# Optimization experiments

Measured on AMD Instinct MI355X. Metric: run time of the kernel, lower is better.

Reference implementation:

```python
import jax, jax.numpy as jnp
import numpy as np

N = 100000      # nodes
E = 1600000     # edges
G = 64          # graphs in batch
IN_CH = 2
HID = 64
HEADS = 4
TASKS = 2
NEG_SLOPE = 0.2  # PyG GATConv default leaky-relu slope


def gat_conv(x, src, dst, W, att_src, att_dst, bias, heads, out_ch, concat):
    """PyG-style GATConv (eval mode, self-loops added).
    x: [N, F_in]; src/dst: [Et]; W: [F_in, heads*out_ch];
    att_src/att_dst: [heads, out_ch]; bias: [heads*out_ch] or [out_ch]."""
    n = x.shape[0]
    xh = (x @ W).reshape(n, heads, out_ch)            # [N,H,C]
    a_src = jnp.einsum('nhc,hc->nh', xh, att_src)     # [N,H]
    a_dst = jnp.einsum('nhc,hc->nh', xh, att_dst)     # [N,H]
    e = a_src[src] + a_dst[dst]                       # [Et,H]
    e = jax.nn.leaky_relu(e, NEG_SLOPE)
    # segment softmax over incoming edges of each destination node
    e_max = jax.ops.segment_max(e, dst, num_segments=n)
    alpha = jnp.exp(e - e_max[dst])
    denom = jax.ops.segment_sum(alpha, dst, num_segments=n)
    alpha = alpha / denom[dst]                        # [Et,H]
    msg = xh[src] * alpha[:, :, None]                 # [Et,H,C]
    out = jax.ops.segment_sum(msg, dst, num_segments=n)  # [N,H,C]
    if concat:
        return out.reshape(n, heads * out_ch) + bias
    return out.mean(axis=1) + bias


def setup_inputs() -> dict:
    key = jax.random.key(0)
    ks = jax.random.split(key, 13)
    s = 0.1
    return {
        'x': jax.random.normal(ks[0], (N, IN_CH), dtype=jnp.float32),
        'edge_index': jax.random.randint(ks[1], (2, E), 0, N, dtype=jnp.int64)
            if jax.config.jax_enable_x64 else jax.random.randint(ks[1], (2, E), 0, N, dtype=jnp.int32),
        'batch': jnp.sort(jax.random.randint(ks[2], (N,), 0, G, dtype=jnp.int32)),
        'W1': jax.random.normal(ks[3], (IN_CH, HEADS * HID), dtype=jnp.float32) * s,
        'att_src1': jax.random.normal(ks[4], (HEADS, HID), dtype=jnp.float32) * s,
        'att_dst1': jax.random.normal(ks[5], (HEADS, HID), dtype=jnp.float32) * s,
        'b1': jnp.zeros((HEADS * HID,), dtype=jnp.float32),
        'W2': jax.random.normal(ks[6], (HEADS * HID, HID), dtype=jnp.float32) * s,
        'att_src2': jax.random.normal(ks[7], (1, HID), dtype=jnp.float32) * s,
        'att_dst2': jax.random.normal(ks[8], (1, HID), dtype=jnp.float32) * s,
        'b2': jnp.zeros((HID,), dtype=jnp.float32),
        'W_lin': jax.random.normal(ks[9], (HID, TASKS), dtype=jnp.float32) * s,
        'b_lin': jnp.zeros((TASKS,), dtype=jnp.float32),
    }


def reference(x, edge_index, batch, W1, att_src1, att_dst1, b1,
              W2, att_src2, att_dst2, b2, W_lin, b_lin):
    n = x.shape[0]
    # PyG GATConv adds self-loops by default
    loops = jnp.arange(n, dtype=edge_index.dtype)
    src = jnp.concatenate([edge_index[0], loops])
    dst = jnp.concatenate([edge_index[1], loops])

    h = jax.nn.elu(gat_conv(x, src, dst, W1, att_src1, att_dst1, b1,
                            HEADS, HID, concat=True))        # [N, 256]
    # dropout is identity in eval mode
    h = jax.nn.elu(gat_conv(h, src, dst, W2, att_src2, att_dst2, b2,
                            1, HID, concat=False))           # [N, 64]

    # global mean pool over graphs
    sums = jax.ops.segment_sum(h, batch, num_segments=G)     # [G, 64]
    counts = jax.ops.segment_sum(jnp.ones((n,), h.dtype), batch, num_segments=G)
    pooled = sums / jnp.maximum(counts, 1.0)[:, None]

    return pooled @ W_lin + b_lin                            # [G, 2]
```

## Files before the change

### kernel.cpp

```cpp
#include <hip/hip_runtime.h>
#include <hip/hip_fp16.h>
#include <math.h>

#define HID 64
#define HEADS 4
#define GR 64
#define NEG 0.2f
#define NBKT_MAX 512
#define BK_SH 8
#define PART_T 2048

typedef _Float16 f16x8 __attribute__((ext_vector_type(8)));
typedef float    f32x4 __attribute__((ext_vector_type(4)));

__device__ __forceinline__ float lrelu(float v){ return v > 0.f ? v : NEG * v; }
__device__ __forceinline__ float elu_(float v){ return v > 0.f ? v : __expf(v) - 1.f; }

__global__ void k_init(float* sums, int* counts, int* bcnt,
                       const float* __restrict__ W1, const float* __restrict__ as1,
                       const float* __restrict__ ad1, float* cvec){
    int i = blockIdx.x * blockDim.x + threadIdx.x;
    if (i < GR * HID) sums[i] = 0.f;
    if (i < GR) counts[i] = 0;
    if (i < NBKT_MAX) bcnt[i] = 0;
    if (blockIdx.x == 0 && threadIdx.x < 64){
        int lane = threadIdx.x;
#pragma unroll
        for (int h = 0; h < HEADS; h++){
            int j = h * HID + lane;
            float s0 = W1[j]       * as1[j];
            float s1 = W1[256 + j] * as1[j];
            float d0 = W1[j]       * ad1[j];
            float d1 = W1[256 + j] * ad1[j];
#pragma unroll
            for (int off = 32; off; off >>= 1){
                s0 += __shfl_xor(s0, off, 64);
                s1 += __shfl_xor(s1, off, 64);
                d0 += __shfl_xor(d0, off, 64);
                d1 += __shfl_xor(d1, off, 64);
            }
            if (lane == 0){
                cvec[h] = s0; cvec[4 + h] = s1; cvec[8 + h] = d0; cvec[12 + h] = d1;
            }
        }
    }
}

__global__ void k_histW(const int* __restrict__ dst, int E, int* bcnt,
                        const float* __restrict__ W2, uint4* __restrict__ w2frag){
    __shared__ int bh[NBKT_MAX];
    if (blockIdx.x < 256){
        for (int b = threadIdx.x; b < NBKT_MAX; b += blockDim.x) bh[b] = 0;
        __syncthreads();
        int stride = 256 * blockDim.x;
        for (int i = blockIdx.x * blockDim.x + threadIdx.x; i < E; i += stride)
            atomicAdd(&bh[dst[i] >> BK_SH], 1);
        __syncthreads();
        for (int b = threadIdx.x; b < NBKT_MAX; b += blockDim.x)
            if (bh[b]) atomicAdd(&bcnt[b], bh[b]);
    } else {
        int t = (blockIdx.x - 256) * 256 + threadIdx.x;
        if (t < 2048){
            int lane = t & 63, c = (t >> 6) & 3, s = t >> 8;
            union { uint4 u; _Float16 h[8]; } o;
#pragma unroll
            for (int e = 0; e < 8; e++){
                int k = 32 * s + 4 * (lane >> 4) + (e & 3) + 16 * (e >> 2);
                int col = 16 * c + (lane & 15);
                o.h[e] = (_Float16)W2[k * 64 + col];
            }
            w2frag[t] = o.u;
        }
    }
}

__global__ void k_bscan(const int* __restrict__ bcnt, int* bbase, int* bcursor){
    __shared__ int sh[NBKT_MAX];
    int t = threadIdx.x;
    int v = bcnt[t];
    sh[t] = v;
    __syncthreads();
    for (int off = 1; off < NBKT_MAX; off <<= 1){
        int u = (t >= off) ? sh[t - off] : 0;
        __syncthreads();
        sh[t] += u;
        __syncthreads();
    }
    bbase[t] = sh[t] - v;
    bcursor[t] = sh[t] - v;
    if (t == NBKT_MAX - 1) bbase[NBKT_MAX] = sh[t];
}

__global__ void __launch_bounds__(256)
k_part(const int* __restrict__ src, const int* __restrict__ dst, int E,
       int* bcursor, unsigned int* __restrict__ tmp){
    __shared__ int bh[NBKT_MAX];
    __shared__ int gbl[NBKT_MAX];
    int tid = threadIdx.x;
    int base = blockIdx.x * PART_T;
    for (int b = tid; b < NBKT_MAX; b += 256) bh[b] = 0;
    __syncthreads();
#pragma unroll
    for (int r = 0; r < PART_T / 256; r++){
        int i = base + r * 256 + tid;
        if (i < E) atomicAdd(&bh[dst[i] >> BK_SH], 1);
    }
    __syncthreads();
    for (int b = tid; b < NBKT_MAX; b += 256){
        int c = bh[b];
        gbl[b] = c ? atomicAdd(&bcursor[b], c) : 0;
        bh[b] = 0;
    }
    __syncthreads();
#pragma unroll
    for (int r = 0; r < PART_T / 256; r++){
        int i = base + r * 256 + tid;
        if (i < E){
            int s = src[i], d = dst[i];
            int b = d >> BK_SH;
            int rank = atomicAdd(&bh[b], 1);
            tmp[(size_t)(gbl[b] + rank)] =
                ((unsigned)(d & ((1 << BK_SH) - 1)) << 17) | (unsigned)s;
        }
    }
}

__global__ void __launch_bounds__(256)
k_csr2(const unsigned int* __restrict__ tmp, const int* __restrict__ bbase,
       int N, int Et, int* __restrict__ offs, int* __restrict__ ssrc){
    __shared__ int degl[256];
    __shared__ int rc[256];
    __shared__ int scan[256];
    __shared__ int ofl[256];
    int b = blockIdx.x, tid = threadIdx.x;
    int n0 = b << BK_SH;
    int nloc = min(256, N - n0);
    degl[tid] = 0; rc[tid] = 0;
    __syncthreads();
    int beg = bbase[b], cnt = bbase[b + 1] - beg;
    for (int i = tid; i < cnt; i += 256)
        atomicAdd(&degl[tmp[beg + i] >> 17], 1);
    __syncthreads();
    int v = (tid < nloc) ? degl[tid] + 1 : 0;
    scan[tid] = v;
    __syncthreads();
    for (int off = 1; off < 256; off <<= 1){
        int u = (tid >= off) ? scan[tid - off] : 0;
        __syncthreads();
        scan[tid] += u;
        __syncthreads();
    }
    int base = beg + n0;
    if (tid < nloc){
        int o = base + scan[tid] - v;
        ofl[tid] = o;
        offs[n0 + tid] = o;
        ssrc[o] = n0 + tid;
    }
    if (b == 0 && tid == 0) offs[N] = Et;
    __syncthreads();
    for (int i = tid; i < cnt; i += 256){
        unsigned int e = tmp[beg + i];
        int dloc = (int)(e >> 17);
        int s = (int)(e & 0x1FFFFu);
        int pos = ofl[dloc] + 1 + atomicAdd(&rc[dloc], 1);
        ssrc[pos] = s;
    }
}

__global__ void k_agg1s(const float* __restrict__ x, const int* __restrict__ offs,
                        const int* __restrict__ ssrc, const float* __restrict__ cvec,
                        int N, float4* Sa, float4* Sb, float4* Sc){
    int t = blockIdx.x * blockDim.x + threadIdx.x;
    int n = t >> 2, sub = t & 3;
    if (n >= N) return;
    float4 cs0 = ((const float4*)cvec)[0];
    float4 cs1 = ((const float4*)cvec)[1];
    float4 cd0 = ((const float4*)cvec)[2];
    float4 cd1 = ((const float4*)cvec)[3];
    float c0[4] = {cs0.x, cs0.y, cs0.z, cs0.w};
    float c1[4] = {cs1.x, cs1.y, cs1.z, cs1.w};
    float2 xn = ((const float2*)x)[n];
    float ad[4] = {xn.x*cd0.x + xn.y*cd1.x, xn.x*cd0.y + xn.y*cd1.y,
                   xn.x*cd0.z + xn.y*cd1.z, xn.x*cd0.w + xn.y*cd1.w};
    float A0[4] = {0,0,0,0}, A1[4] = {0,0,0,0}, D[4] = {0,0,0,0};
    int beg = offs[n], end = offs[n + 1];
    int j = beg + sub;
    for (; j + 12 < end; j += 16){
        int si[4] = {ssrc[j], ssrc[j+4], ssrc[j+8], ssrc[j+12]};
        float2 xs[4];
#pragma unroll
        for (int u = 0; u < 4; u++) xs[u] = ((const float2*)x)[si[u]];
#pragma unroll
        for (int h = 0; h < HEADS; h++){
#pragma unroll
            for (int u = 0; u < 4; u++){
                float w = __expf(lrelu(xs[u].x * c0[h] + xs[u].y * c1[h] + ad[h]));
                A0[h] += w * xs[u].x;
                A1[h] += w * xs[u].y;
                D[h]  += w;
            }
        }
    }
    for (; j < end; j += 4){
        int s = ssrc[j];
        float2 xs = ((const float2*)x)[s];
#pragma unroll
        for (int h = 0; h < HEADS; h++){
            float e = xs.x * c0[h] + xs.y * c1[h] + ad[h];
            float w = __expf(lrelu(e));
            A0[h] += w * xs.x;
            A1[h] += w * xs.y;
            D[h]  += w;
        }
    }
#pragma unroll
    for (int h = 0; h < HEADS; h++){
        A0[h] += __shfl_xor(A0[h], 1, 64); A0[h] += __shfl_xor(A0[h], 2, 64);
        A1[h] += __shfl_xor(A1[h], 1, 64); A1[h] += __shfl_xor(A1[h], 2, 64);
        D[h]  += __shfl_xor(D[h],  1, 64); D[h]  += __shfl_xor(D[h],  2, 64);
    }
    if (sub == 0){
        Sa[n] = make_float4(A0[0], A0[1], A0[2], A0[3]);
        Sb[n] = make_float4(A1[0], A1[1], A1[2], A1[3]);
        Sc[n] = make_float4(D[0],  D[1],  D[2],  D[3]);
    }
}

__global__ void __launch_bounds__(256)
k_mfma(const float4* __restrict__ Sa4, const float4* __restrict__ Sb4,
       const float4* __restrict__ Sc4, const float* __restrict__ W1,
       const float* __restrict__ b1, const uint4* __restrict__ w2frag,
       const float* __restrict__ as2, const float* __restrict__ ad2,
       int N, __half* __restrict__ xh2, float* __restrict__ asrc,
       float* __restrict__ adst){
    __shared__ uint4 w2s[2048];
    __shared__ float4 w1aS[64], w1bS[64], b1S[64];
    int tid = threadIdx.x;
    for (int i = tid; i < 2048; i += 256) w2s[i] = w2frag[i];
    if (tid < 64){
        w1aS[tid] = ((const float4*)W1)[tid];
        w1bS[tid] = ((const float4*)W1)[tid + 64];
        b1S[tid]  = ((const float4*)b1)[tid];
    }
    __syncthreads();

    int lane = tid & 63, wv = tid >> 6;
    int r = lane & 15, g = lane >> 4;
    float asw0 = as2[r], asw1 = as2[16 + r], asw2 = as2[32 + r], asw3 = as2[48 + r];
    float adw0 = ad2[r], adw1 = ad2[16 + r], adw2 = ad2[32 + r], adw3 = ad2[48 + r];

    int ntiles = (N + 15) >> 4;
    for (int t = blockIdx.x * 4 + wv; t < ntiles; t += gridDim.x * 4){
        int base = t << 4;
        int nodeA = min(base + r, N - 1);
        float4 sa = Sa4[nodeA], sb = Sb4[nodeA], sc = Sc4[nodeA];
        float rdv0 = 1.0f / sc.x, rdv1 = 1.0f / sc.y;
        float rdv2 = 1.0f / sc.z, rdv3 = 1.0f / sc.w;
        f32x4 ac0 = {0.f,0.f,0.f,0.f}, ac1 = {0.f,0.f,0.f,0.f};
        f32x4 ac2 = {0.f,0.f,0.f,0.f}, ac3 = {0.f,0.f,0.f,0.f};
#pragma unroll
        for (int s = 0; s < 8; s++){
            const int head = s >> 1;
            float A0 = head == 0 ? sa.x : head == 1 ? sa.y : head == 2 ? sa.z : sa.w;
            float A1 = head == 0 ? sb.x : head == 1 ? sb.y : head == 2 ? sb.z : sb.w;
            float rd = head == 0 ? rdv0 : head == 1 ? rdv1 : head == 2 ? rdv2 : rdv3;
            int q0 = 8 * s + g;
            float4 w0lo = w1aS[q0], w0hi = w1aS[q0 + 4];
            float4 w1lo = w1bS[q0], w1hi = w1bS[q0 + 4];
            float4 blo  = b1S[q0],  bhi  = b1S[q0 + 4];
            union { uint4 u; f16x8 f; _Float16 h[8]; } a;
            a.h[0] = (_Float16)elu_((A0 * w0lo.x + A1 * w1lo.x) * rd + blo.x);
            a.h[1] = (_Float16)elu_((A0 * w0lo.y + A1 * w1lo.y) * rd + blo.y);
            a.h[2] = (_Float16)elu_((A0 * w0lo.z + A1 * w1lo.z) * rd + blo.z);
            a.h[3] = (_Float16)elu_((A0 * w0lo.w + A1 * w1lo.w) * rd + blo.w);
            a.h[4] = (_Float16)elu_((A0 * w0hi.x + A1 * w1hi.x) * rd + bhi.x);
            a.h[5] = (_Float16)elu_((A0 * w0hi.y + A1 * w1hi.y) * rd + bhi.y);
            a.h[6] = (_Float16)elu_((A0 * w0hi.z + A1 * w1hi.z) * rd + bhi.z);
            a.h[7] = (_Float16)elu_((A0 * w0hi.w + A1 * w1hi.w) * rd + bhi.w);
            union { uint4 u; f16x8 f; } b0, b1x, b2, b3;
            b0.u  = w2s[(s * 4 + 0) * 64 + lane];
            b1x.u = w2s[(s * 4 + 1) * 64 + lane];
            b2.u  = w2s[(s * 4 + 2) * 64 + lane];
            b3.u  = w2s[(s * 4 + 3) * 64 + lane];
            ac0 = __builtin_amdgcn_mfma_f32_16x16x32_f16(a.f, b0.f,  ac0, 0, 0, 0);
            ac1 = __builtin_amdgcn_mfma_f32_16x16x32_f16(a.f, b1x.f, ac1, 0, 0, 0);
            ac2 = __builtin_amdgcn_mfma_f32_16x16x32_f16(a.f, b2.f,  ac2, 0, 0, 0);
            ac3 = __builtin_amdgcn_mfma_f32_16x16x32_f16(a.f, b3.f,  ac3, 0, 0, 0);
        }
        float ps0 = 0.f, ps1 = 0.f, ps2 = 0.f, ps3 = 0.f;
        float pd0 = 0.f, pd1 = 0.f, pd2 = 0.f, pd3 = 0.f;
#pragma unroll
        for (int reg = 0; reg < 4; reg++){
            int node = base + 4 * g + reg;
            if (node < N){
                size_t rowb = (size_t)node * 64;
                xh2[rowb +      r] = __float2half(ac0[reg]);
                xh2[rowb + 16 + r] = __float2half(ac1[reg]);
                xh2[rowb + 32 + r] = __float2half(ac2[reg]);
                xh2[rowb + 48 + r] = __float2half(ac3[reg]);
            }
            float ps = ac0[reg]*asw0 + ac1[reg]*asw1 + ac2[reg]*asw2 + ac3[reg]*asw3;
            float pd = ac0[reg]*adw0 + ac1[reg]*adw1 + ac2[reg]*adw2 + ac3[reg]*adw3;
            if (reg == 0){ ps0 = ps; pd0 = pd; }
            else if (reg == 1){ ps1 = ps; pd1 = pd; }
            else if (reg == 2){ ps2 = ps; pd2 = pd; }
            else { ps3 = ps; pd3 = pd; }
        }
#pragma unroll
        for (int m = 1; m < 16; m <<= 1){
            ps0 += __shfl_xor(ps0, m, 64); pd0 += __shfl_xor(pd0, m, 64);
            ps1 += __shfl_xor(ps1, m, 64); pd1 += __shfl_xor(pd1, m, 64);
            ps2 += __shfl_xor(ps2, m, 64); pd2 += __shfl_xor(pd2, m, 64);
            ps3 += __shfl_xor(ps3, m, 64); pd3 += __shfl_xor(pd3, m, 64);
        }
        if (r == 0){
            int nb = base + 4 * g;
            if (nb     < N){ asrc[nb    ] = ps0; adst[nb    ] = pd0; }
            if (nb + 1 < N){ asrc[nb + 1] = ps1; adst[nb + 1] = pd1; }
            if (nb + 2 < N){ asrc[nb + 2] = ps2; adst[nb + 2] = pd2; }
            if (nb + 3 < N){ asrc[nb + 3] = ps3; adst[nb + 3] = pd3; }
        }
    }
}

__global__ void k_agg2p(const __half* __restrict__ xh2, const float* __restrict__ asrc,
                        const float* __restrict__ adst, const int* __restrict__ offs,
                        const int* __restrict__ ssrc, const float* __restrict__ b2,
                        const int* __restrict__ batch, int N,
                        float* sums, int* counts){
    int tid = threadIdx.x;
    int lane = tid & 63, wv = tid >> 6;
    int c = lane & 31;
    int half = lane >> 5;
    int l16 = lane & 15;
    int wid = blockIdx.x * 4 + wv;
    int nw = gridDim.x * 4;
    int chunk = (N + nw - 1) / nw;
    int beg = wid * chunk, end = min(beg + chunk, N);
    if (beg >= end) return;
    const unsigned int* xrow = (const unsigned int*)xh2;
    float b2a = b2[2 * c], b2b = b2[2 * c + 1];
    float pacc0 = 0.f, pacc1 = 0.f; int pcnt = 0; int cur = batch[beg];
    for (int n = beg; n < end; n++){
        float ad = adst[n];
        float acc0 = 0.f, acc1 = 0.f, den = 0.f;
        int e0 = offs[n], e1 = offs[n + 1];
        int j = e0;
        for (; j + 16 <= e1; j += 16){
            int sA = ssrc[j + l16];
            float wA = __expf(lrelu(asrc[sA] + ad));
            int su[8];
#pragma unroll
            for (int u = 0; u < 8; u++) su[u] = __shfl(sA, 2 * u + half, 64);
            unsigned int rv[8];
#pragma unroll
            for (int u = 0; u < 8; u++) rv[u] = xrow[(size_t)su[u] * 32 + c];
#pragma unroll
            for (int u = 0; u < 8; u++){
                float wu = __shfl(wA, 2 * u + half, 64);
                float2 f = __half22float2(*(const __half2*)&rv[u]);
                acc0 += wu * f.x;
                acc1 += wu * f.y;
                den  += wu;
            }
        }
        if (j + 8 <= e1){
            int sA = ssrc[j + (lane & 7)];
            float wA = __expf(lrelu(asrc[sA] + ad));
            int su[4];
#pragma unroll
            for (int u = 0; u < 4; u++) su[u] = __shfl(sA, 2 * u + half, 64);
            unsigned int rv[4];
#pragma unroll
            for (int u = 0; u < 4; u++) rv[u] = xrow[(size_t)su[u] * 32 + c];
#pragma unroll
            for (int u = 0; u < 4; u++){
                float wu = __shfl(wA, 2 * u + half, 64);
                float2 f = __half22float2(*(const __half2*)&rv[u]);
                acc0 += wu * f.x;
                acc1 += wu * f.y;
                den  += wu;
            }
            j += 8;
        }
        for (; j + 2 <= e1; j += 2){
            int s = ssrc[j + half];
            float a = asrc[s];
            unsigned int rr = xrow[(size_t)s * 32 + c];
            float w = __expf(lrelu(a + ad));
            float2 f = __half22float2(*(const __half2*)&rr);
            acc0 += w * f.x;
            acc1 += w * f.y;
            den  += w;
        }
        if (j < e1){
            int s = ssrc[j];
            float w = (half == 0) ? __expf(lrelu(asrc[s] + ad)) : 0.f;
            unsigned int rr = xrow[(size_t)s * 32 + c];
            float2 f = __half22float2(*(const __half2*)&rr);
            acc0 += w * f.x;
            acc1 += w * f.y;
            den  += w;
        }
        acc0 += __shfl_xor(acc0, 32, 64);
        acc1 += __shfl_xor(acc1, 32, 64);
        den  += __shfl_xor(den, 32, 64);
        float h2a = elu_(acc0 / den + b2a);
        float h2b = elu_(acc1 / den + b2b);
        int g = batch[n];
        if (g != cur){
            if (half == 0){
                atomicAdd(&sums[cur * HID + 2 * c    ], pacc0);
                atomicAdd(&sums[cur * HID + 2 * c + 1], pacc1);
            }
            if (lane == 0) atomicAdd(&counts[cur], pcnt);
            pacc0 = 0.f; pacc1 = 0.f; pcnt = 0; cur = g;
        }
        pacc0 += h2a; pacc1 += h2b; pcnt++;
    }
    if (half == 0){
        atomicAdd(&sums[cur * HID + 2 * c    ], pacc0);
        atomicAdd(&sums[cur * HID + 2 * c + 1], pacc1);
    }
    if (lane == 0) atomicAdd(&counts[cur], pcnt);
}

__global__ void k_final(const float* __restrict__ sums, const int* __restrict__ counts,
                        const float* __restrict__ Wl, const float* __restrict__ bl,
                        float* out){
    int t = threadIdx.x;
    if (t >= GR * 2) return;
    int g = t >> 1, task = t & 1;
    float c = (float)max(counts[g], 1);
    float acc = 0.f;
#pragma unroll
    for (int k = 0; k < HID; k++)
        acc += (sums[g * HID + k] / c) * Wl[k * 2 + task];
    out[t] = acc + bl[task];
}

extern "C" void kernel_launch(void* const* d_in, const int* in_sizes, int n_in,
                              void* d_out, int out_size, void* d_ws, size_t ws_size,
                              hipStream_t stream) {
    const float* x    = (const float*)d_in[0];
    const int*   ei   = (const int*)  d_in[1];
    const int*   batch= (const int*)  d_in[2];
    const float* W1   = (const float*)d_in[3];
    const float* as1  = (const float*)d_in[4];
    const float* ad1  = (const float*)d_in[5];
    const float* b1   = (const float*)d_in[6];
    const float* W2   = (const float*)d_in[7];
    const float* as2  = (const float*)d_in[8];
    const float* ad2  = (const float*)d_in[9];
    const float* b2   = (const float*)d_in[10];
    const float* Wl   = (const float*)d_in[11];
    const float* bl   = (const float*)d_in[12];
    float* out = (float*)d_out;

    int N  = in_sizes[0] / 2;
    int E  = in_sizes[1] / 2;
    int Et = E + N;
    const int* srcp = ei;
    const int* dstp = ei + E;

    char* p = (char*)d_ws;
    auto alloc = [&](size_t bytes)->char* {
        char* r = p; p += (bytes + 255) & ~(size_t)255; return r;
    };
    int*    offs   = (int*)   alloc((size_t)(N + 1) * 4);
    int*    bcnt   = (int*)   alloc(NBKT_MAX * 4);
    int*    bbase  = (int*)   alloc((NBKT_MAX + 1) * 4);
    int*    bcursor= (int*)   alloc(NBKT_MAX * 4);
    int*    ssrc   = (int*)   alloc((size_t)Et * 4);
    unsigned int* tmp = (unsigned int*)alloc((size_t)E * 4);
    float*  cvec   = (float*) alloc(16 * 4);
    float4* Sa     = (float4*)alloc((size_t)N * 16);
    float4* Sb     = (float4*)alloc((size_t)N * 16);
    float4* Sc     = (float4*)alloc((size_t)N * 16);
    float*  asrc2  = (float*) alloc((size_t)N * 4);
    float*  adst2  = (float*) alloc((size_t)N * 4);
    float*  sums   = (float*) alloc((size_t)GR * HID * 4);
    int*    counts = (int*)   alloc((size_t)GR * 4);
    uint4*  w2frag = (uint4*) alloc(2048 * 16);
    __half* xh2    = (__half*)alloc((size_t)N * 64 * 2);

    int nbkt = (N + 255) >> BK_SH;

    k_init <<<16, 256, 0, stream>>>(sums, counts, bcnt, W1, as1, ad1, cvec);
    k_histW<<<264, 256, 0, stream>>>(dstp, E, bcnt, W2, w2frag);
    k_bscan<<<1, NBKT_MAX, 0, stream>>>(bcnt, bbase, bcursor);
    k_part <<<(E + PART_T - 1) / PART_T, 256, 0, stream>>>(srcp, dstp, E, bcursor, tmp);
    k_csr2 <<<nbkt, 256, 0, stream>>>(tmp, bbase, N, Et, offs, ssrc);

    k_agg1s<<<((N * 4) + 255) / 256, 256, 0, stream>>>(x, offs, ssrc, cvec, N, Sa, Sb, Sc);
    k_mfma <<<1024, 256, 0, stream>>>(Sa, Sb, Sc, W1, b1, w2frag, as2, ad2,
                                      N, xh2, asrc2, adst2);
    k_agg2p<<<2048, 256, 0, stream>>>(xh2, asrc2, adst2, offs, ssrc, b2,
                                      batch, N, sums, counts);
    k_final<<<1, 128, 0, stream>>>(sums, counts, Wl, bl, out);
}
```

Measured before the change: 216.0 us.

## Prefetch next node's neighbor indices and issue fixed 32-edge gather in layer-2 aggregation

Restructures the layer-2 aggregation loop so each wave software-pipelines: the source indices for the next destination node are loaded while the current node's features and attention scores are gathered. The variable-length 16/8/2 edge loops are replaced by a fixed 16-slot-per-half-wave unrolled gather covering up to 32 edges, with masked slots pointing at a valid dummy row, plus a scalar tail loop for larger degrees. The aim is to hide the dependent index-then-row gather latency and raise memory-level parallelism. The cost is more registers, which may lower occupancy, and wasted loads for nodes with fewer than 32 incoming edges (average degree is about 17).

After: 212.7 us. About the same (-1.5%).

```diff
diff --git a/kernel.cpp b/kernel.cpp
--- a/kernel.cpp
+++ b/kernel.cpp
@@ -333,7 +333,6 @@
     int lane = tid & 63, wv = tid >> 6;
     int c = lane & 31;
     int half = lane >> 5;
-    int l16 = lane & 15;
     int wid = blockIdx.x * 4 + wv;
     int nw = gridDim.x * 4;
     int chunk = (N + nw - 1) / nw;
@@ -342,66 +341,61 @@
     const unsigned int* xrow = (const unsigned int*)xh2;
     float b2a = b2[2 * c], b2b = b2[2 * c + 1];
     float pacc0 = 0.f, pacc1 = 0.f; int pcnt = 0; int cur = batch[beg];
+
+    int e0 = offs[beg], e1 = offs[beg + 1];
+    int idxv[16];
+#pragma unroll
+    for (int u = 0; u < 16; u++){
+        int j = e0 + 2 * u + half;
+        idxv[u] = (j < e1) ? ssrc[j] : beg;
+    }
     for (int n = beg; n < end; n++){
+        int e2 = (n + 1 < end) ? offs[n + 2] : e1;
         float ad = adst[n];
+        float av[16];
+        unsigned int rv[16];
+#pragma unroll
+        for (int u = 0; u < 16; u++){
+            av[u] = asrc[idxv[u]];
+            rv[u] = xrow[(size_t)idxv[u] * 32 + c];
+        }
+        int nidxv[16];
+#pragma unroll
+        for (int u = 0; u < 16; u++) nidxv[u] = 0;
+        if (n + 1 < end){
+#pragma unroll
+            for (int u = 0; u < 16; u++){
+                int j = e1 + 2 * u + half;
+                nidxv[u] = (j < e2) ? ssrc[j] : (n + 1);
+            }
+        }
         float acc0 = 0.f, acc1 = 0.f, den = 0.f;
-        int e0 = offs[n], e1 = offs[n + 1];
-        int j = e0;
-        for (; j + 16 <= e1; j += 16){
-            int sA = ssrc[j + l16];
-            float wA = __expf(lrelu(asrc[sA] + ad));
-            int su[8];
-#pragma unroll
-            for (int u = 0; u < 8; u++) su[u] = __shfl(sA, 2 * u + half, 64);
-            unsigned int rv[8];
-#pragma unroll
-            for (int u = 0; u < 8; u++) rv[u] = xrow[(size_t)su[u] * 32 + c];
-#pragma unroll
-            for (int u = 0; u < 8; u++){
-                float wu = __shfl(wA, 2 * u + half, 64);
-                float2 f = __half22float2(*(const __half2*)&rv[u]);
-                acc0 += wu * f.x;
-                acc1 += wu * f.y;
-                den  += wu;
-            }
-        }
-        if (j + 8 <= e1){
-            int sA = ssrc[j + (lane & 7)];
-            float wA = __expf(lrelu(asrc[sA] + ad));
-            int su[4];
-#pragma unroll
-            for (int u = 0; u < 4; u++) su[u] = __shfl(sA, 2 * u + half, 64);
-            unsigned int rv[4];
-#pragma unroll
-            for (int u = 0; u < 4; u++) rv[u] = xrow[(size_t)su[u] * 32 + c];
-#pragma unroll
-            for (int u = 0; u < 4; u++){
-                float wu = __shfl(wA, 2 * u + half, 64);
-                float2 f = __half22float2(*(const __half2*)&rv[u]);
-                acc0 += wu * f.x;
-                acc1 += wu * f.y;
-                den  += wu;
-            }
-            j += 8;
-        }
-        for (; j + 2 <= e1; j += 2){
-            int s = ssrc[j + half];
-            float a = asrc[s];
-            unsigned int rr = xrow[(size_t)s * 32 + c];
-            float w = __expf(lrelu(a + ad));
-            float2 f = __half22float2(*(const __half2*)&rr);
+#pragma unroll
+        for (int u = 0; u < 16; u++){
+            bool v = (e0 + 2 * u + half) < e1;
+            float w = v ? __expf(lrelu(av[u] + ad)) : 0.f;
+            float2 f = __half22float2(*(const __half2*)&rv[u]);
             acc0 += w * f.x;
             acc1 += w * f.y;
             den  += w;
         }
-        if (j < e1){
-            int s = ssrc[j];
-            float w = (half == 0) ? __expf(lrelu(asrc[s] + ad)) : 0.f;
-            unsigned int rr = xrow[(size_t)s * 32 + c];
-            float2 f = __half22float2(*(const __half2*)&rr);
-            acc0 += w * f.x;
-            acc1 += w * f.y;
-            den  += w;
+        if (e1 - e0 > 32){
+            int j = e0 + 32;
+            for (; j + 2 <= e1; j += 2){
+                int s = ssrc[j + half];
+                float a = asrc[s];
+                unsigned int rr = xrow[(size_t)s * 32 + c];
+                float w = __expf(lrelu(a + ad));
+                float2 f = __half22float2(*(const __half2*)&rr);
+                acc0 += w * f.x; acc1 += w * f.y; den += w;
+            }
+            if (j < e1){
+                int s = ssrc[j];
+                float w = (half == 0) ? __expf(lrelu(asrc[s] + ad)) : 0.f;
+                unsigned int rr = xrow[(size_t)s * 32 + c];
+                float2 f = __half22float2(*(const __half2*)&rr);
+                acc0 += w * f.x; acc1 += w * f.y; den += w;
+            }
         }
         acc0 += __shfl_xor(acc0, 32, 64);
         acc1 += __shfl_xor(acc1, 32, 64);
@@ -418,6 +412,9 @@
             pacc0 = 0.f; pacc1 = 0.f; pcnt = 0; cur = g;
         }
         pacc0 += h2a; pacc1 += h2b; pcnt++;
+        e0 = e1; e1 = e2;
+#pragma unroll
+        for (int u = 0; u < 16; u++) idxv[u] = nidxv[u];
     }
     if (half == 0){
         atomicAdd(&sums[cur * HID + 2 * c    ], pacc0);
```
